# Performance work log

Hardware: AMD Instinct MI355X
Metric: run time of the kernel (lower is better)

The kernel has to match this reference:

```python
import jax, jax.numpy as jnp
import numpy as np

ALPHA = 0.2      # LeakyReLU negative slope
NEG_INF = -9e15  # mask value from the original module
EPS = 1e-8


def setup_inputs() -> dict:
    key = jax.random.key(0)
    k1, k2, k3, k4 = jax.random.split(key, 4)
    B, N, F_in, F_out = 8, 2048, 128, 64
    h = jax.random.normal(k1, (B, N, F_in), dtype=jnp.float32)
    u = jax.random.uniform(k2, (B, N, N), dtype=jnp.float32)
    adj = jnp.where(u > 0.9, u, 0.0)
    adj = jnp.maximum(adj, jnp.eye(N, dtype=jnp.float32)[None])
    # Xavier-uniform with gain 1.414 as in the torch init
    gain = 1.414
    bW = gain * np.sqrt(6.0 / (F_in + F_out))
    W = jax.random.uniform(k3, (F_in, F_out), jnp.float32, -bW, bW)
    ba = gain * np.sqrt(6.0 / (2 * F_out + 1))
    a = jax.random.uniform(k4, (2 * F_out, 1), jnp.float32, -ba, ba)
    return {"h": h, "adj": adj, "W": W, "a": a}


def reference(h, adj, W, a):
    # h: [B,N,Fin], adj: [B,N,N], W: [Fin,Fout], a: [2*Fout,1]
    F_out = W.shape[1]
    Wh = jnp.einsum('bnf,fo->bno', h, W)                      # [B,N,Fout]
    # Split-projection equivalent of cat([Wh_i, Wh_j]) @ a:
    # e[b,i,j] = leaky(Wh[b,i]@a1 + Wh[b,j]@a2)
    a1 = a[:F_out, 0]
    a2 = a[F_out:, 0]
    e = jax.nn.leaky_relu(
        (Wh @ a1)[:, :, None] + (Wh @ a2)[:, None, :],        # [B,N,N]
        negative_slope=ALPHA,
    )
    att = jnp.where(adj > 0, e, NEG_INF)
    att = jax.nn.softmax(att, axis=2)
    att = att * adj
    att = att / (jnp.sum(att, axis=2, keepdims=True) + EPS)
    h_prime = jnp.einsum('bij,bjo->bio', att, Wh)             # [B,N,Fout]
    return jax.nn.elu(h_prime)                                # concat=True -> ELU
```

## Files before the change

### kernel.cpp

```cpp
#include <hip/hip_runtime.h>
#include <hip/hip_bf16.h>
#include <stdint.h>

#define LRELU_ALPHA 0.2f

constexpr int BB = 8, NN = 2048, FIN = 128, FOUT = 64;
constexpr int GEMM_ROWS = 32;
constexpr int NBLK_G = BB * NN / GEMM_ROWS;

typedef __attribute__((ext_vector_type(8))) short short8;
typedef __attribute__((ext_vector_type(4))) float f32x4;

__device__ __forceinline__ ushort bf16rn(float f) {
    __hip_bfloat16 h = __float2bfloat16(f);
    return *reinterpret_cast<ushort*>(&h);
}

#define HS 132
__global__ __launch_bounds__(256) void k_gemm_hw(const float* __restrict__ h,
                                                 const float* __restrict__ W,
                                                 const float* __restrict__ a,
                                                 ushort* __restrict__ WhP,
                                                 float* __restrict__ s1,
                                                 float* __restrict__ s2,
                                                 float* __restrict__ pmax) {
    __shared__ float hs[GEMM_ROWS * HS];
    __shared__ __align__(16) ushort fragbuf[2048];
    __shared__ float smax[16];
    const int tid = threadIdx.x;
    const int base = blockIdx.x * GEMM_ROWS;

    #pragma unroll
    for (int rep = 0; rep < 4; ++rep) {
        int flat4 = rep * 256 + tid;
        int row = flat4 >> 5, k4 = flat4 & 31;
        float4 v = *reinterpret_cast<const float4*>(h + (size_t)(base + row) * FIN + k4 * 4);
        *reinterpret_cast<float4*>(&hs[row * HS + k4 * 4]) = v;
    }
    __syncthreads();

    const int tr = tid >> 4;
    const int tc = tid & 15;
    float acc[2][4] = {};
    #pragma unroll 4
    for (int k = 0; k < FIN; ++k) {
        float4 wv = *reinterpret_cast<const float4*>(W + (size_t)k * FOUT + tc * 4);
        #pragma unroll
        for (int r = 0; r < 2; ++r) {
            float hv = hs[(tr * 2 + r) * HS + k];
            acc[r][0] = fmaf(hv, wv.x, acc[r][0]);
            acc[r][1] = fmaf(hv, wv.y, acc[r][1]);
            acc[r][2] = fmaf(hv, wv.z, acc[r][2]);
            acc[r][3] = fmaf(hv, wv.w, acc[r][3]);
        }
    }

    #pragma unroll
    for (int r = 0; r < 2; ++r) {
        const int jloc = tr * 2 + r;
        const int e = jloc & 7, kgrp = jloc >> 3;
        #pragma unroll
        for (int c = 0; c < 4; ++c) {
            const int col = tc * 4 + c;
            fragbuf[((col >> 4) * 64 + kgrp * 16 + (col & 15)) * 8 + e] = bf16rn(acc[r][c]);
        }
    }

    float a1c[4], a2c[4];
    #pragma unroll
    for (int c = 0; c < 4; ++c) {
        a1c[c] = a[tc * 4 + c];
        a2c[c] = a[FOUT + tc * 4 + c];
    }
    float maxp2 = -3.4e38f;
    #pragma unroll
    for (int r = 0; r < 2; ++r) {
        float p1 = acc[r][0] * a1c[0] + acc[r][1] * a1c[1] + acc[r][2] * a1c[2] + acc[r][3] * a1c[3];
        float p2 = acc[r][0] * a2c[0] + acc[r][1] * a2c[1] + acc[r][2] * a2c[2] + acc[r][3] * a2c[3];
        #pragma unroll
        for (int off = 1; off < 16; off <<= 1) {
            p1 += __shfl_xor(p1, off);
            p2 += __shfl_xor(p2, off);
        }
        if (tc == 0) {
            s1[base + tr * 2 + r] = p1;
            s2[base + tr * 2 + r] = p2;
            maxp2 = fmaxf(maxp2, p2);
        }
    }
    if (tc == 0) smax[tr] = maxp2;
    __syncthreads();

    const size_t region = ((size_t)((base >> 11) * 64 + ((base & 2047) >> 5))) * 2048;
    *reinterpret_cast<uint4*>(WhP + region + tid * 8) =
        *reinterpret_cast<const uint4*>(fragbuf + tid * 8);

    if (tid == 0) {
        float mm = smax[0];
        #pragma unroll
        for (int i = 1; i < 16; ++i) mm = fmaxf(mm, smax[i]);
        pmax[blockIdx.x] = mm;
    }
}

__global__ __launch_bounds__(256, 4) void k_attn(const float* __restrict__ adj,
                                                 const ushort* __restrict__ WhP,
                                                 const float* __restrict__ s1,
                                                 const float* __restrict__ s2,
                                                 const float* __restrict__ pmax,
                                                 float* __restrict__ out) {
    __shared__ float2 e2buf[NN];
    __shared__ float lacc[4][16][68];
    __shared__ float lS[4][16];

    const int tid = threadIdx.x;
    const int l = tid & 63, w = tid >> 6;
    const int li = l & 15, lk = l >> 4;
    const int blk = blockIdx.x;
    const int b = blk >> 7;
    const int rowbase = blk * 16;
    const int row_i = rowbase + li;

    float m = -3.4e38f;
    #pragma unroll
    for (int t = 0; t < 8; ++t) m = fmaxf(m, pmax[l + 64 * t]);
    #pragma unroll
    for (int off = 32; off > 0; off >>= 1) m = fmaxf(m, __shfl_xor(m, off));

    const float* __restrict__ s2B = s2 + (size_t)b * NN;
    #pragma unroll
    for (int k = 0; k < 8; ++k) {
        const int j = k * 256 + tid;
        const float d = s2B[j] - m;
        e2buf[j] = make_float2(__expf(d), __expf(LRELU_ALPHA * d));
    }

    const float s1i = s1[row_i];
    const float cp = s1i + m;
    const float e1p = __expf(0.8f * fminf(cp, 0.f));
    const float e1n = __expf(-0.8f * fmaxf(cp, 0.f));

    __syncthreads();

    const float* __restrict__ adjp = adj + (size_t)row_i * NN + w * 512 + lk * 8;
    const ushort* __restrict__ whp = WhP + (size_t)b * 131072 + (size_t)(w * 16) * 2048 + l * 8;
    const float2* __restrict__ e2w = e2buf + w * 512 + lk * 8;

    f32x4 acc0 = {0.f, 0.f, 0.f, 0.f};
    f32x4 acc1 = {0.f, 0.f, 0.f, 0.f};
    f32x4 acc2 = {0.f, 0.f, 0.f, 0.f};
    f32x4 acc3 = {0.f, 0.f, 0.f, 0.f};
    f32x4 accS = {0.f, 0.f, 0.f, 0.f};
    short8 ones;
    #pragma unroll
    for (int e = 0; e < 8; ++e) ones[e] = (short)0x3F80;

    float4 a0 = *reinterpret_cast<const float4*>(adjp);
    float4 a1 = *reinterpret_cast<const float4*>(adjp + 4);
    short8 b0 = *reinterpret_cast<const short8*>(whp);
    short8 b1 = *reinterpret_cast<const short8*>(whp + 512);
    short8 b2 = *reinterpret_cast<const short8*>(whp + 1024);
    short8 b3 = *reinterpret_cast<const short8*>(whp + 1536);

    #pragma unroll 2
    for (int t = 0; t < 16; ++t) {
        const int tn = (t < 15) ? t + 1 : 15;
        float4 na0 = *reinterpret_cast<const float4*>(adjp + tn * 32);
        float4 na1 = *reinterpret_cast<const float4*>(adjp + tn * 32 + 4);
        const ushort* np = whp + tn * 2048;
        short8 nb0 = *reinterpret_cast<const short8*>(np);
        short8 nb1 = *reinterpret_cast<const short8*>(np + 512);
        short8 nb2 = *reinterpret_cast<const short8*>(np + 1024);
        short8 nb3 = *reinterpret_cast<const short8*>(np + 1536);

        const float4* e2q = reinterpret_cast<const float4*>(e2w + t * 32);
        const float4 q0 = e2q[0], q1 = e2q[1], q2 = e2q[2], q3 = e2q[3];

        uint32_t u0, u1, pk0, pk1, pk2, pk3;
#define WV(AV, P2, N2) (__float_as_uint((AV) * fmaxf(e1p * (P2), e1n * (N2))) + 0x8000u)
        u0 = WV(a0.x, q0.x, q0.y); u1 = WV(a0.y, q0.z, q0.w);
        pk0 = __builtin_amdgcn_perm(u1, u0, 0x07060302);
        u0 = WV(a0.z, q1.x, q1.y); u1 = WV(a0.w, q1.z, q1.w);
        pk1 = __builtin_amdgcn_perm(u1, u0, 0x07060302);
        u0 = WV(a1.x, q2.x, q2.y); u1 = WV(a1.y, q2.z, q2.w);
        pk2 = __builtin_amdgcn_perm(u1, u0, 0x07060302);
        u0 = WV(a1.z, q3.x, q3.y); u1 = WV(a1.w, q3.z, q3.w);
        pk3 = __builtin_amdgcn_perm(u1, u0, 0x07060302);
#undef WV
        int4 afw = make_int4((int)pk0, (int)pk1, (int)pk2, (int)pk3);
        short8 af = *reinterpret_cast<short8*>(&afw);

        acc0 = __builtin_amdgcn_mfma_f32_16x16x32_bf16(af, b0, acc0, 0, 0, 0);
        acc1 = __builtin_amdgcn_mfma_f32_16x16x32_bf16(af, b1, acc1, 0, 0, 0);
        acc2 = __builtin_amdgcn_mfma_f32_16x16x32_bf16(af, b2, acc2, 0, 0, 0);
        acc3 = __builtin_amdgcn_mfma_f32_16x16x32_bf16(af, b3, acc3, 0, 0, 0);
        accS = __builtin_amdgcn_mfma_f32_16x16x32_bf16(af, ones, accS, 0, 0, 0);

        a0 = na0; a1 = na1;
        b0 = nb0; b1 = nb1; b2 = nb2; b3 = nb3;
    }

    if (li == 0) {
        #pragma unroll
        for (int r = 0; r < 4; ++r) lS[w][lk * 4 + r] = accS[r];
    }
    #pragma unroll
    for (int r = 0; r < 4; ++r) {
        lacc[w][lk * 4 + r][0 * 16 + li] = acc0[r];
        lacc[w][lk * 4 + r][1 * 16 + li] = acc1[r];
        lacc[w][lk * 4 + r][2 * 16 + li] = acc2[r];
        lacc[w][lk * 4 + r][3 * 16 + li] = acc3[r];
    }
    __syncthreads();

    #pragma unroll
    for (int q = 0; q < 4; ++q) {
        const int idx = q * 256 + tid;
        const int row = idx >> 6, col = idx & 63;
        float v = lacc[0][row][col] + lacc[1][row][col] + lacc[2][row][col] + lacc[3][row][col];
        float S = lS[0][row] + lS[1][row] + lS[2][row] + lS[3][row];
        float o = v / S;
        o = o > 0.f ? o : expm1f(o);
        out[(size_t)(rowbase + row) * FOUT + col] = o;
    }
}

extern "C" void kernel_launch(void* const* d_in, const int* in_sizes, int n_in,
                              void* d_out, int out_size, void* d_ws, size_t ws_size,
                              hipStream_t stream) {
    (void)in_sizes; (void)n_in; (void)out_size; (void)ws_size;
    const float* h   = (const float*)d_in[0];
    const float* adj = (const float*)d_in[1];
    const float* W   = (const float*)d_in[2];
    const float* a   = (const float*)d_in[3];
    float* out = (float*)d_out;

    ushort* WhP = (ushort*)d_ws;
    float* s1w  = (float*)(WhP + (size_t)BB * NN * FOUT);
    float* s2w  = s1w + (size_t)BB * NN;
    float* pmaxw = s2w + (size_t)BB * NN;

    k_gemm_hw<<<NBLK_G, 256, 0, stream>>>(h, W, a, WhP, s1w, s2w, pmaxw);
    k_attn<<<BB * NN / 16, 256, 0, stream>>>(adj, WhP, s1w, s2w, pmaxw, out);
}
```

Measured before the change: 45.58 us.

## Split attention over two column halves and merge partial sums in extra kernel

The attention kernel now splits each 16-row block's neighbour range into two halves of 1024 columns, doubling the grid to 2048 blocks. Each half writes an unnormalised partial accumulator and row sum to workspace (half 0) or to the output buffer (half 1). A new merge kernel adds the two partials, normalises and applies ELU. The aim is more parallelism and occupancy on the adjacency stream, at the cost of an extra launch and an extra round trip of partial results through global memory.

```diff
diff --git a/kernel.cpp b/kernel.cpp
--- a/kernel.cpp
+++ b/kernel.cpp
@@ -7,6 +7,7 @@
 constexpr int BB = 8, NN = 2048, FIN = 128, FOUT = 64;
 constexpr int GEMM_ROWS = 32;
 constexpr int NBLK_G = BB * NN / GEMM_ROWS;
+constexpr int JH = 1024;
 
 typedef __attribute__((ext_vector_type(8))) short short8;
 typedef __attribute__((ext_vector_type(4))) float f32x4;
@@ -108,17 +109,21 @@
                                                  const float* __restrict__ s1,
                                                  const float* __restrict__ s2,
                                                  const float* __restrict__ pmax,
+                                                 float* __restrict__ pacc,
+                                                 float* __restrict__ pS0,
+                                                 float* __restrict__ pS1,
                                                  float* __restrict__ out) {
-    __shared__ float2 e2buf[NN];
+    __shared__ float2 e2buf[JH];
     __shared__ float lacc[4][16][68];
     __shared__ float lS[4][16];
 
     const int tid = threadIdx.x;
     const int l = tid & 63, w = tid >> 6;
     const int li = l & 15, lk = l >> 4;
-    const int blk = blockIdx.x;
-    const int b = blk >> 7;
-    const int rowbase = blk * 16;
+    const int p = blockIdx.x >> 10;
+    const int g = blockIdx.x & 1023;
+    const int b = g >> 7;
+    const int rowbase = g * 16;
     const int row_i = rowbase + li;
 
     float m = -3.4e38f;
@@ -127,9 +132,9 @@
     #pragma unroll
     for (int off = 32; off > 0; off >>= 1) m = fmaxf(m, __shfl_xor(m, off));
 
-    const float* __restrict__ s2B = s2 + (size_t)b * NN;
-    #pragma unroll
-    for (int k = 0; k < 8; ++k) {
+    const float* __restrict__ s2B = s2 + (size_t)b * NN + p * JH;
+    #pragma unroll
+    for (int k = 0; k < 4; ++k) {
         const int j = k * 256 + tid;
         const float d = s2B[j] - m;
         e2buf[j] = make_float2(__expf(d), __expf(LRELU_ALPHA * d));
@@ -142,9 +147,9 @@
 
     __syncthreads();
 
-    const float* __restrict__ adjp = adj + (size_t)row_i * NN + w * 512 + lk * 8;
-    const ushort* __restrict__ whp = WhP + (size_t)b * 131072 + (size_t)(w * 16) * 2048 + l * 8;
-    const float2* __restrict__ e2w = e2buf + w * 512 + lk * 8;
+    const float* __restrict__ adjp = adj + (size_t)row_i * NN + p * JH + w * 256 + lk * 8;
+    const ushort* __restrict__ whp = WhP + (size_t)b * 131072 + (size_t)(p * 32 + w * 8) * 2048 + l * 8;
+    const float2* __restrict__ e2w = e2buf + w * 256 + lk * 8;
 
     f32x4 acc0 = {0.f, 0.f, 0.f, 0.f};
     f32x4 acc1 = {0.f, 0.f, 0.f, 0.f};
@@ -163,8 +168,8 @@
     short8 b3 = *reinterpret_cast<const short8*>(whp + 1536);
 
     #pragma unroll 2
-    for (int t = 0; t < 16; ++t) {
-        const int tn = (t < 15) ? t + 1 : 15;
+    for (int t = 0; t < 8; ++t) {
+        const int tn = (t < 7) ? t + 1 : 7;
         float4 na0 = *reinterpret_cast<const float4*>(adjp + tn * 32);
         float4 na1 = *reinterpret_cast<const float4*>(adjp + tn * 32 + 4);
         const ushort* np = whp + tn * 2048;
@@ -219,9 +224,30 @@
         const int row = idx >> 6, col = idx & 63;
         float v = lacc[0][row][col] + lacc[1][row][col] + lacc[2][row][col] + lacc[3][row][col];
         float S = lS[0][row] + lS[1][row] + lS[2][row] + lS[3][row];
+        if (p == 0) {
+            pacc[(size_t)g * 1024 + idx] = v;
+            if (col == 0) pS0[g * 16 + row] = S;
+        } else {
+            out[(size_t)g * 1024 + idx] = v;
+            if (col == 0) pS1[g * 16 + row] = S;
+        }
+    }
+}
+
+__global__ __launch_bounds__(256) void k_merge(const float* __restrict__ pacc,
+                                               const float* __restrict__ pS0,
+                                               const float* __restrict__ pS1,
+                                               float* __restrict__ out) {
+    const int tid = threadIdx.x;
+    #pragma unroll
+    for (int q = 0; q < 4; ++q) {
+        const size_t idx = (size_t)blockIdx.x * 1024 + q * 256 + tid;
+        const int row = (int)(idx >> 6);
+        float v = pacc[idx] + out[idx];
+        float S = pS0[row] + pS1[row];
         float o = v / S;
         o = o > 0.f ? o : expm1f(o);
-        out[(size_t)(rowbase + row) * FOUT + col] = o;
+        out[idx] = o;
     }
 }
 
@@ -239,7 +265,12 @@
     float* s1w  = (float*)(WhP + (size_t)BB * NN * FOUT);
     float* s2w  = s1w + (size_t)BB * NN;
     float* pmaxw = s2w + (size_t)BB * NN;
+    float* pacc = pmaxw + NBLK_G;
+    float* pS0  = pacc + (size_t)BB * NN * FOUT;
+    float* pS1  = pS0 + (size_t)BB * NN;
 
     k_gemm_hw<<<NBLK_G, 256, 0, stream>>>(h, W, a, WhP, s1w, s2w, pmaxw);
-    k_attn<<<BB * NN / 16, 256, 0, stream>>>(adj, WhP, s1w, s2w, pmaxw, out);
-}
+    k_attn<<<2 * BB * NN / 16, 256, 0, stream>>>(adj, WhP, s1w, s2w, pmaxw,
+                                                 pacc, pS0, pS1, out);
+    k_merge<<<BB * NN * FOUT / 1024, 256, 0, stream>>>(pacc, pS0, pS1, out);
+}
```

Result: slower. 51.44 us (+12.9%).
